# Kernel optimization log

Hardware: AMD Instinct MI355X
Metric: run time of the kernel (lower is better)

## Reference

```python
import jax, jax.numpy as jnp
import numpy as np

B, N, K, TC = 4, 4096, 16, 3
N_TAYLOR = 20  # 3rd-order Taylor monomials of (x,y,z): 1 + 3 + 6 + 10
CHANNELS = [(6, 32), (32, 64), (64, 128), (128, 256)]


def _taylor(rel):
    # rel: B,3,N,K relative coords -> B,20,N,K monomial basis up to degree 3
    x, y, z = rel[:, 0], rel[:, 1], rel[:, 2]
    one = jnp.ones_like(x)
    return jnp.stack([one, x, y, z,
                      x * x, x * y, x * z, y * y, y * z, z * z,
                      x * x * x, x * x * y, x * x * z, x * y * y, x * y * z,
                      x * z * z, y * y * y, y * y * z, y * z * z, z * z * z], axis=1)


def _group(feat, idx):
    # feat: B,C,N ; idx: B,N,K (int) -> B,C,N,K gathered neighbor features
    return jax.vmap(lambda f, i: f[:, i])(feat, idx)


def setup_inputs() -> dict:
    key = jax.random.key(0)
    ks = jax.random.split(key, 8)
    inp = {"pc": jax.random.normal(ks[0], (B, N, 6), dtype=jnp.float32)}
    for l, (cin, cout) in enumerate(CHANNELS, start=1):
        k1, k2 = jax.random.split(ks[l], 2)
        inp[f"w1_{l}"] = jax.random.normal(k1, (TC, N_TAYLOR), dtype=jnp.float32) * 0.1
        inp[f"b1_{l}"] = jnp.zeros((TC,), dtype=jnp.float32)
        fan_in = cin * TC * K
        inp[f"w2_{l}"] = jax.random.normal(k2, (cout, cin * TC, K), dtype=jnp.float32) * (1.0 / np.sqrt(fan_in))
        inp[f"b2_{l}"] = jnp.zeros((cout,), dtype=jnp.float32)
    return inp


def _forward(pc, params):
    pcT = pc.transpose(0, 2, 1)                 # B,6,N
    xyz = pcT[:, :3]                            # B,3,N
    # KNN graph: pairwise squared distances, top-k nearest (includes self)
    sq = jnp.sum(xyz * xyz, axis=1)             # B,N
    d2 = sq[:, :, None] + sq[:, None, :] - 2.0 * jnp.einsum('bcn,bcm->bnm', xyz, xyz)
    _, idx = jax.lax.top_k(-d2, K)              # B,N,K
    gxyz = _group(xyz, idx)                     # B,3,N,K
    rel = gxyz - xyz[:, :, :, None]             # B,3,N,K relative neighbor coords
    tay_basis = _taylor(rel)                    # B,20,N,K

    feat = pcT
    feats = []
    for (w1, b1, w2, b2) in params:
        # Taylor kernel weights: 1x1 conv over the 20 monomials -> TC channels
        tay = jnp.einsum('btnk,ct->bcnk', tay_basis, w1) + b1[None, :, None, None]  # B,TC,N,K
        gf = _group(feat, idx)                  # B,C,N,K
        C = gf.shape[1]
        fused = (gf[:, :, None] * tay[:, None]).reshape(B, C * TC, N, K)  # outer product
        # Conv2d(C*TC, out, kernel=(1,K)): contract channel and neighbor axes
        out = jnp.einsum('bcnk,ock->bon', fused, w2) + b2[None, :, None]
        feat = jax.nn.relu(out)                 # B,Cout,N
        feats.append(feat)

    point_feat = jnp.concatenate(feats, axis=1)  # B,480,N
    top2, _ = jax.lax.top_k(point_feat, 2)       # top-2 over N (last axis) -> B,480,2
    cat_feat = top2.reshape(B, -1)               # B,960
    return cat_feat, point_feat


def reference(pc, w1_1, b1_1, w2_1, b2_1, w1_2, b1_2, w2_2, b2_2,
              w1_3, b1_3, w2_3, b2_3, w1_4, b1_4, w2_4, b2_4):
    params = [(w1_1, b1_1, w2_1, b2_1), (w1_2, b1_2, w2_2, b2_2),
              (w1_3, b1_3, w2_3, b2_3), (w1_4, b1_4, w2_4, b2_4)]
    return _forward(pc, params)
```

## Files before the change

### kernel.cpp

```cpp
#include <hip/hip_runtime.h>
#include <hip/hip_fp16.h>
#include <cfloat>

#define BB 4
#define NN 4096
#define KK 16
#define NPTS (BB * NN)
#define NT48 (48 * NPTS)

typedef __attribute__((ext_vector_type(8))) _Float16 f16x8;
typedef __attribute__((ext_vector_type(4))) float f32x4;
typedef unsigned int u32;
typedef unsigned long long u64;

__device__ __forceinline__ short f2h(float v) {
  __half h = __float2half_rn(v);
  return __half_as_short(h);
}
__device__ __forceinline__ u32 mulh2(u32 a, __half2 t) {
  __half2 x = __hmul2(*(__half2*)&a, t);
  return *(u32*)&x;
}

__global__ __launch_bounds__(256) void pc2ft_kernel(const float* __restrict__ pc,
                                                    short* __restrict__ ft0,
                                                    float4* __restrict__ xyzq) {
  const int i = blockIdx.x * 256 + threadIdx.x;
  if (i >= NPTS) return;
  const float* s = pc + (size_t)i * 6;
  short* d = ft0 + (size_t)i * 8;
#pragma unroll
  for (int c = 0; c < 6; ++c) d[c] = f2h(s[c]);
  d[6] = 0; d[7] = 0;
  const float x = s[0], y = s[1], z = s[2];
  xyzq[i] = make_float4(x, y, z, fmaf(z, z, fmaf(y, y, x * x)));
}

__global__ __launch_bounds__(256) void knn_select(const float4* __restrict__ xyzq,
                                                  int* __restrict__ idx_out) {
  __shared__ float wT[4];
  __shared__ u64 list[128];
  __shared__ int lcnt;
  const int g = blockIdx.x;
  const int b = g >> 12;
  const int t = threadIdx.x;
  const int lane = t & 63;
  const float4* base = xyzq + (b << 12);
  const float4 q = xyzq[g];
  float d2v[16];
  float mymin = FLT_MAX;
#pragma unroll
  for (int i = 0; i < 16; ++i) {
    const float4 c = base[i * 256 + t];
    const float dot = fmaf(q.z, c.z, fmaf(q.y, c.y, q.x * c.x));
    d2v[i] = fmaf(-2.0f, dot, q.w + c.w);
    mymin = fminf(mymin, d2v[i]);
  }
  if (t == 0) lcnt = 0;
  float v = mymin;
#pragma unroll
  for (int k = 2; k <= 64; k <<= 1) {
#pragma unroll
    for (int j = k >> 1; j >= 1; j >>= 1) {
      const float o = __shfl_xor(v, j, 64);
      const bool take_min = (((lane & k) == 0) == ((lane & j) == 0));
      v = take_min ? fminf(v, o) : fmaxf(v, o);
    }
  }
  const float tw = __shfl(v, 15, 64);
  if (lane == 0) wT[t >> 6] = tw;
  __syncthreads();
  const float T = fminf(fminf(wT[0], wT[1]), fminf(wT[2], wT[3]));
#pragma unroll
  for (int i = 0; i < 16; ++i) {
    if (d2v[i] <= T) {
      const u32 bits = __float_as_uint(d2v[i]);
      const u32 key = bits ^ ((u32)((int)bits >> 31) | 0x80000000u);
      const int pos = atomicAdd(&lcnt, 1);
      if (pos < 128) list[pos] = ((u64)key << 32) | (u32)(i * 256 + t);
    }
  }
  __syncthreads();
  if (t < 128) {
    const int m = min(lcnt, 128);
    const u64 my = (t < m) ? list[t] : ~0ull;
    int rank = 0;
#pragma unroll 4
    for (int i = 0; i < m; ++i) rank += (list[i] < my) ? 1 : 0;
    if (t < m && rank < 16)
      idx_out[(size_t)g * KK + rank] = (int)(my & 0xFFFFFFFFull);
  }
}

__global__ __launch_bounds__(256) void wcvt_kernel(const float* __restrict__ w2,
                                                   short* __restrict__ wb,
                                                   int CIN, int COUT, int CPAD, int LOGC,
                                                   int total8) {
  const int i = blockIdx.x * 256 + threadIdx.x;
  if (i >= total8) return;
  const int q8 = i * 8;
  const int QT = CPAD * 48;
  const int o = q8 / QT;
  const int r = q8 - o * QT;
  const int kq = r >> LOGC;
  const int c0 = r & (CPAD - 1);
  const int tt = kq >> 4;
  const int k = kq & 15;
  short h[8];
#pragma unroll
  for (int j = 0; j < 8; ++j) {
    const int c = c0 + j;
    const float v = (o < COUT && c < CIN) ? w2[(size_t)o * CIN * 48 + (c * 3 + tt) * 16 + k] : 0.0f;
    h[j] = f2h(v);
  }
  short* d = wb + (size_t)o * QT + r;
#pragma unroll
  for (int j = 0; j < 8; ++j) d[j] = h[j];
}

__global__ __launch_bounds__(256) void taylor_kernel(
    const float* __restrict__ pc, const int* __restrict__ idx,
    const float* __restrict__ w1_1, const float* __restrict__ b1_1,
    const float* __restrict__ w1_2, const float* __restrict__ b1_2,
    const float* __restrict__ w1_3, const float* __restrict__ b1_3,
    const float* __restrict__ w1_4, const float* __restrict__ b1_4,
    float* __restrict__ tayg) {
  const int i = blockIdx.x * 256 + threadIdx.x;
  if (i >= NPTS * KK) return;
  const int p = i & (NPTS - 1);
  const int k = i >> 14;
  const int n = p & (NN - 1);
  const int b = p >> 12;
  const float* pcb = pc + (size_t)b * NN * 6;
  const int m = idx[(size_t)p * KK + k];
  const float x = pcb[m * 6 + 0] - pcb[n * 6 + 0];
  const float y = pcb[m * 6 + 1] - pcb[n * 6 + 1];
  const float z = pcb[m * 6 + 2] - pcb[n * 6 + 2];
  float tb[20];
  tb[0] = 1.0f; tb[1] = x; tb[2] = y; tb[3] = z;
  tb[4] = x * x; tb[5] = x * y; tb[6] = x * z;
  tb[7] = y * y; tb[8] = y * z; tb[9] = z * z;
  tb[10] = tb[4] * x; tb[11] = tb[4] * y; tb[12] = tb[4] * z;
  tb[13] = tb[5] * y; tb[14] = tb[5] * z; tb[15] = tb[6] * z;
  tb[16] = tb[7] * y; tb[17] = tb[7] * z; tb[18] = tb[8] * z; tb[19] = tb[9] * z;
  const float* w1s[4] = {w1_1, w1_2, w1_3, w1_4};
  const float* b1s[4] = {b1_1, b1_2, b1_3, b1_4};
#pragma unroll
  for (int l = 0; l < 4; ++l) {
    const float* w1 = w1s[l];
    const float* b1 = b1s[l];
#pragma unroll
    for (int c = 0; c < 3; ++c) {
      float s = b1[c];
#pragma unroll
      for (int j = 0; j < 20; ++j) s = fmaf(w1[c * 20 + j], tb[j], s);
      tayg[(size_t)(l * 48 + c * 16 + k) * NPTS + p] = s;
    }
  }
}

template <int CPAD, int LOGC, int COUT, int OTILE>
__global__ __launch_bounds__(256) void conv_mfma_kernel(
    const char* __restrict__ ftin,
    const short* __restrict__ wb,
    const float* __restrict__ b2,
    const float* __restrict__ tayg,
    const int* __restrict__ idx,
    float* __restrict__ pfout, int pfbstride,
    short* __restrict__ ftout, int CPADN) {
  constexpr int QTOT = CPAD * 48;
  constexpr int STEPS = QTOT / 32;
  constexpr int NJ = OTILE / 64;
  constexpr int PW = 16 * NJ;
  __shared__ __align__(16) short As[2][OTILE * 32];
  __shared__ __align__(16) short Bs[2][64 * 32];
  __shared__ __align__(16) float tayS[48 * 64];
  __shared__ int idxS[16 * 64];
  const int t = threadIdx.x;
  const int pbase = blockIdx.x * 64;
  const int obase = blockIdx.y * OTILE;
  const int b = pbase >> 12;
  const int nbase = pbase & (NN - 1);
  const int p_loc = t >> 2;
  const int sub = t & 3;
#pragma unroll
  for (int i = 0; i < 3; ++i) {
    const int f = i * 1024 + t * 4;
    *(float4*)&tayS[f] = *(const float4*)&tayg[(size_t)(f >> 6) * NPTS + pbase + (f & 63)];
  }
  {
    const int4 mi = *(const int4*)&idx[(size_t)(pbase + p_loc) * KK + sub * 4];
    const int gb = b << 12;
    idxS[(sub * 4 + 0) * 64 + p_loc] = (gb + mi.x) << (LOGC + 1);
    idxS[(sub * 4 + 1) * 64 + p_loc] = (gb + mi.y) << (LOGC + 1);
    idxS[(sub * 4 + 2) * 64 + p_loc] = (gb + mi.z) << (LOGC + 1);
    idxS[(sub * 4 + 3) * 64 + p_loc] = (gb + mi.w) << (LOGC + 1);
  }
  const int lane = t & 63;
  const int w = t >> 6;
  const int wm = (NJ == 2) ? (w & 1) : 0;
  const int wn = (NJ == 2) ? (w >> 1) : w;
  const int fr = lane & 15;
  const int fk = lane >> 4;
  const short* aw = wb + (size_t)(obase + p_loc) * QTOT + sub * 8;
  f32x4 acc[4][NJ];
#pragma unroll
  for (int i = 0; i < 4; ++i)
#pragma unroll
    for (int j = 0; j < NJ; ++j) acc[i][j] = (f32x4)(0.0f);
  __syncthreads();

  uint4 fv[2];
  float tv[2];
  auto pref = [&](int ss, int slot) {
    const int seg = ss * 32 + sub * 8;
    const int kq = seg >> LOGC;
    const int c0 = seg & (CPAD - 1);
    const int moff = idxS[(kq & 15) * 64 + p_loc];
    tv[slot] = tayS[kq * 64 + p_loc];
    fv[slot] = *(const uint4*)(ftin + moff + (c0 << 1));
  };
  auto build = [&](int slot, int dstph) {
    const __half2 t2 = __half2half2(__float2half_rn(tv[slot]));
    const uint4 f = fv[slot];
    uint4 r;
    r.x = mulh2(f.x, t2); r.y = mulh2(f.y, t2);
    r.z = mulh2(f.z, t2); r.w = mulh2(f.w, t2);
    const int chunk = sub ^ ((p_loc >> 1) & 3);
    *(uint4*)&Bs[dstph][p_loc * 32 + chunk * 8] = r;
  };
  auto dmaA = [&](int ss, int dstph) {
#pragma unroll
    for (int h = 0; h < NJ; ++h)
      __builtin_amdgcn_global_load_lds(
          (const __attribute__((address_space(1))) u32*)(aw + (size_t)h * 64 * QTOT + ss * 32),
          (__attribute__((address_space(3))) u32*)&As[dstph][h * 2048 + t * 8], 16, 0, 0);
  };
  pref(0, 0);
  dmaA(0, 0);
  pref(1, 1);
  build(0, 0);
  __syncthreads();
#pragma unroll 2
  for (int s = 0; s < STEPS; ++s) {
    const int ph = s & 1;
    if (s + 2 < STEPS) pref(s + 2, s & 1);
    if (s + 1 < STEPS) dmaA(s + 1, ph ^ 1);
    f16x8 af[4];
#pragma unroll
    for (int i = 0; i < 4; ++i)
      af[i] = *(const f16x8*)&As[ph][(wm * 64 + i * 16 + fr) * 32 + fk * 8];
    f16x8 bfr[NJ];
    const int bch = (fk ^ ((fr >> 1) & 3)) * 8;
#pragma unroll
    for (int j = 0; j < NJ; ++j)
      bfr[j] = *(const f16x8*)&Bs[ph][(wn * PW + j * 16 + fr) * 32 + bch];
    if (s + 1 < STEPS) build((s + 1) & 1, ph ^ 1);
#pragma unroll
    for (int i = 0; i < 4; ++i)
#pragma unroll
      for (int j = 0; j < NJ; ++j)
        acc[i][j] = __builtin_amdgcn_mfma_f32_16x16x32_f16(af[i], bfr[j], acc[i][j], 0, 0, 0);
    if (s + 1 < STEPS) __syncthreads();
  }
  float* outb = pfout + (size_t)b * pfbstride;
#pragma unroll
  for (int i = 0; i < 4; ++i) {
    const int o0 = obase + wm * 64 + i * 16 + fk * 4;
    if (o0 < COUT) {
      const float4 b4 = *(const float4*)&b2[o0];
#pragma unroll
      for (int j = 0; j < NJ; ++j) {
        const int p_l = wn * PW + j * 16 + fr;
        const float v0 = fmaxf(acc[i][j][0] + b4.x, 0.0f);
        const float v1 = fmaxf(acc[i][j][1] + b4.y, 0.0f);
        const float v2 = fmaxf(acc[i][j][2] + b4.z, 0.0f);
        const float v3 = fmaxf(acc[i][j][3] + b4.w, 0.0f);
        outb[(size_t)(o0 + 0) * NN + nbase + p_l] = v0;
        outb[(size_t)(o0 + 1) * NN + nbase + p_l] = v1;
        outb[(size_t)(o0 + 2) * NN + nbase + p_l] = v2;
        outb[(size_t)(o0 + 3) * NN + nbase + p_l] = v3;
        if (ftout) {
          const __half2 h01 = __floats2half2_rn(v0, v1);
          const __half2 h23 = __floats2half2_rn(v2, v3);
          uint2 pk;
          pk.x = *(const u32*)&h01;
          pk.y = *(const u32*)&h23;
          *(uint2*)&ftout[(size_t)(pbase + p_l) * CPADN + o0] = pk;
        }
      }
    }
  }
}

__global__ __launch_bounds__(256) void top2_kernel(const float* __restrict__ pf,
                                                   float* __restrict__ cat) {
  const int row = blockIdx.x;
  const float* p = pf + (size_t)row * NN;
  float m1 = -FLT_MAX, m2 = -FLT_MAX;
  for (int i = threadIdx.x; i < NN; i += 256) {
    const float v = p[i];
    if (v > m1) { m2 = m1; m1 = v; }
    else if (v > m2) m2 = v;
  }
#pragma unroll
  for (int off = 32; off > 0; off >>= 1) {
    const float o1 = __shfl_down(m1, off, 64);
    const float o2 = __shfl_down(m2, off, 64);
    const float nm1 = fmaxf(m1, o1);
    const float nm2 = fmaxf(fminf(m1, o1), fmaxf(m2, o2));
    m1 = nm1; m2 = nm2;
  }
  __shared__ float s1[4], s2[4];
  const int wid = threadIdx.x >> 6;
  if ((threadIdx.x & 63) == 0) { s1[wid] = m1; s2[wid] = m2; }
  __syncthreads();
  if (threadIdx.x == 0) {
    m1 = s1[0]; m2 = s2[0];
#pragma unroll
    for (int w = 1; w < 4; ++w) {
      const float o1 = s1[w], o2 = s2[w];
      const float nm1 = fmaxf(m1, o1);
      const float nm2 = fmaxf(fminf(m1, o1), fmaxf(m2, o2));
      m1 = nm1; m2 = nm2;
    }
    const int b = row / 480, ch = row % 480;
    cat[b * 960 + ch * 2 + 0] = m1;
    cat[b * 960 + ch * 2 + 1] = m2;
  }
}

extern "C" void kernel_launch(void* const* d_in, const int* in_sizes, int n_in,
                              void* d_out, int out_size, void* d_ws, size_t ws_size,
                              hipStream_t stream) {
  const float* pc = (const float*)d_in[0];
  const float* w1s[4]; const float* b1s[4]; const float* w2s[4]; const float* b2s[4];
  for (int l = 0; l < 4; ++l) {
    w1s[l] = (const float*)d_in[1 + 4 * l];
    b1s[l] = (const float*)d_in[2 + 4 * l];
    w2s[l] = (const float*)d_in[3 + 4 * l];
    b2s[l] = (const float*)d_in[4 + 4 * l];
  }
  char* W = (char*)d_ws;
  int* idx = (int*)W;
  float* tayg = (float*)(W + 1048576);
  short* wb1 = (short*)(W + 13631488);
  short* wb2 = wb1 + 64 * 384;
  short* wb3 = wb2 + 64 * 1536;
  short* wb4 = wb3 + 128 * 3072;
  short* ft0 = (short*)(W + 17809408);
  short* ft1 = (short*)(W + 18071552);
  float4* xyzq = (float4*)(W + 1048576);
  short* ft2 = (short*)(W + 1048576);
  short* ft3 = (short*)(W + 1048576 + 2097152);
  float* cat = (float*)d_out;
  float* pf = (float*)d_out + BB * 960;
  const int pfstride = 480 * NN;

  pc2ft_kernel<<<dim3(NPTS / 256), 256, 0, stream>>>(pc, ft0, xyzq);
  knn_select<<<dim3(NPTS), 256, 0, stream>>>(xyzq, idx);
  wcvt_kernel<<<dim3((64 * 384 / 8 + 255) / 256), 256, 0, stream>>>(w2s[0], wb1, 6, 32, 8, 3, 64 * 384 / 8);
  wcvt_kernel<<<dim3((64 * 1536 / 8 + 255) / 256), 256, 0, stream>>>(w2s[1], wb2, 32, 64, 32, 5, 64 * 1536 / 8);
  wcvt_kernel<<<dim3((128 * 3072 / 8 + 255) / 256), 256, 0, stream>>>(w2s[2], wb3, 64, 128, 64, 6, 128 * 3072 / 8);
  wcvt_kernel<<<dim3((256 * 6144 / 8 + 255) / 256), 256, 0, stream>>>(w2s[3], wb4, 128, 256, 128, 7, 256 * 6144 / 8);
  taylor_kernel<<<dim3(NPTS * KK / 256), 256, 0, stream>>>(
      pc, idx, w1s[0], b1s[0], w1s[1], b1s[1], w1s[2], b1s[2], w1s[3], b1s[3], tayg);
  conv_mfma_kernel<8, 3, 32, 64><<<dim3(NPTS / 64, 1), 256, 0, stream>>>(
      (const char*)ft0, wb1, b2s[0], tayg + 0 * (size_t)NT48, idx,
      pf + (size_t)0 * NN, pfstride, ft1, 32);
  conv_mfma_kernel<32, 5, 64, 64><<<dim3(NPTS / 64, 1), 256, 0, stream>>>(
      (const char*)ft1, wb2, b2s[1], tayg + 1 * (size_t)NT48, idx,
      pf + (size_t)32 * NN, pfstride, ft2, 64);
  conv_mfma_kernel<64, 6, 128, 64><<<dim3(NPTS / 64, 2), 256, 0, stream>>>(
      (const char*)ft2, wb3, b2s[2], tayg + 2 * (size_t)NT48, idx,
      pf + (size_t)96 * NN, pfstride, ft3, 128);
  conv_mfma_kernel<128, 7, 256, 128><<<dim3(NPTS / 64, 2), 256, 0, stream>>>(
      (const char*)ft3, wb4, b2s[3], tayg + 3 * (size_t)NT48, idx,
      pf + (size_t)224 * NN, pfstride, nullptr, 0);
  top2_kernel<<<dim3(BB * 480), 256, 0, stream>>>(pf, cat);
}
```

Measured before the change: 377.1 us.

## Feed MFMA operands directly from registers, removing LDS staging and block barriers

New measurement: 600.0 us. 1.59x slower.

```diff
diff --git a/kernel.cpp b/kernel.cpp
--- a/kernel.cpp
+++ b/kernel.cpp
@@ -160,7 +160,7 @@
 }
 
 template <int CPAD, int LOGC, int COUT, int OTILE>
-__global__ __launch_bounds__(256) void conv_mfma_kernel(
+__global__ __launch_bounds__(256) void conv_reg_kernel(
     const char* __restrict__ ftin,
     const short* __restrict__ wb,
     const float* __restrict__ b2,
@@ -172,8 +172,6 @@
   constexpr int STEPS = QTOT / 32;
   constexpr int NJ = OTILE / 64;
   constexpr int PW = 16 * NJ;
-  __shared__ __align__(16) short As[2][OTILE * 32];
-  __shared__ __align__(16) short Bs[2][64 * 32];
   __shared__ __align__(16) float tayS[48 * 64];
   __shared__ int idxS[16 * 64];
   const int t = threadIdx.x;
@@ -181,14 +179,14 @@
   const int obase = blockIdx.y * OTILE;
   const int b = pbase >> 12;
   const int nbase = pbase & (NN - 1);
-  const int p_loc = t >> 2;
-  const int sub = t & 3;
 #pragma unroll
   for (int i = 0; i < 3; ++i) {
     const int f = i * 1024 + t * 4;
     *(float4*)&tayS[f] = *(const float4*)&tayg[(size_t)(f >> 6) * NPTS + pbase + (f & 63)];
   }
   {
+    const int p_loc = t >> 2;
+    const int sub = t & 3;
     const int4 mi = *(const int4*)&idx[(size_t)(pbase + p_loc) * KK + sub * 4];
     const int gb = b << 12;
     idxS[(sub * 4 + 0) * 64 + p_loc] = (gb + mi.x) << (LOGC + 1);
@@ -202,7 +200,11 @@
   const int wn = (NJ == 2) ? (w >> 1) : w;
   const int fr = lane & 15;
   const int fk = lane >> 4;
-  const short* aw = wb + (size_t)(obase + p_loc) * QTOT + sub * 8;
+  const int fkx8 = fk * 8;
+  const short* awbase = wb + (size_t)(obase + wm * 64 + fr) * QTOT + fkx8;
+  int pl[NJ];
+#pragma unroll
+  for (int j = 0; j < NJ; ++j) pl[j] = wn * PW + j * 16 + fr;
   f32x4 acc[4][NJ];
 #pragma unroll
   for (int i = 0; i < 4; ++i)
@@ -210,58 +212,45 @@
     for (int j = 0; j < NJ; ++j) acc[i][j] = (f32x4)(0.0f);
   __syncthreads();
 
-  uint4 fv[2];
-  float tv[2];
-  auto pref = [&](int ss, int slot) {
-    const int seg = ss * 32 + sub * 8;
-    const int kq = seg >> LOGC;
-    const int c0 = seg & (CPAD - 1);
-    const int moff = idxS[(kq & 15) * 64 + p_loc];
-    tv[slot] = tayS[kq * 64 + p_loc];
-    fv[slot] = *(const uint4*)(ftin + moff + (c0 << 1));
+  uint4 areg[2][4];
+  uint4 bfv[2][NJ];
+  float btv[2][NJ];
+  auto loadstep = [&](int s, int slot) {
+    const int q0 = s * 32 + fkx8;
+    const int kq = q0 >> LOGC;
+    const int c0 = q0 & (CPAD - 1);
+#pragma unroll
+    for (int i = 0; i < 4; ++i)
+      areg[slot][i] = *(const uint4*)(awbase + (size_t)i * 16 * QTOT + s * 32);
+#pragma unroll
+    for (int j = 0; j < NJ; ++j) {
+      const int moff = idxS[(kq & 15) * 64 + pl[j]];
+      btv[slot][j] = tayS[kq * 64 + pl[j]];
+      bfv[slot][j] = *(const uint4*)(ftin + moff + (c0 << 1));
+    }
   };
-  auto build = [&](int slot, int dstph) {
-    const __half2 t2 = __half2half2(__float2half_rn(tv[slot]));
-    const uint4 f = fv[slot];
-    uint4 r;
-    r.x = mulh2(f.x, t2); r.y = mulh2(f.y, t2);
-    r.z = mulh2(f.z, t2); r.w = mulh2(f.w, t2);
-    const int chunk = sub ^ ((p_loc >> 1) & 3);
-    *(uint4*)&Bs[dstph][p_loc * 32 + chunk * 8] = r;
-  };
-  auto dmaA = [&](int ss, int dstph) {
-#pragma unroll
-    for (int h = 0; h < NJ; ++h)
-      __builtin_amdgcn_global_load_lds(
-          (const __attribute__((address_space(1))) u32*)(aw + (size_t)h * 64 * QTOT + ss * 32),
-          (__attribute__((address_space(3))) u32*)&As[dstph][h * 2048 + t * 8], 16, 0, 0);
-  };
-  pref(0, 0);
-  dmaA(0, 0);
-  pref(1, 1);
-  build(0, 0);
-  __syncthreads();
+  loadstep(0, 0);
 #pragma unroll 2
   for (int s = 0; s < STEPS; ++s) {
-    const int ph = s & 1;
-    if (s + 2 < STEPS) pref(s + 2, s & 1);
-    if (s + 1 < STEPS) dmaA(s + 1, ph ^ 1);
-    f16x8 af[4];
-#pragma unroll
-    for (int i = 0; i < 4; ++i)
-      af[i] = *(const f16x8*)&As[ph][(wm * 64 + i * 16 + fr) * 32 + fk * 8];
+    const int cur = s & 1;
+    if (s + 1 < STEPS) loadstep(s + 1, cur ^ 1);
     f16x8 bfr[NJ];
-    const int bch = (fk ^ ((fr >> 1) & 3)) * 8;
-#pragma unroll
-    for (int j = 0; j < NJ; ++j)
-      bfr[j] = *(const f16x8*)&Bs[ph][(wn * PW + j * 16 + fr) * 32 + bch];
-    if (s + 1 < STEPS) build((s + 1) & 1, ph ^ 1);
-#pragma unroll
-    for (int i = 0; i < 4; ++i)
+#pragma unroll
+    for (int j = 0; j < NJ; ++j) {
+      const __half2 t2 = __half2half2(__float2half_rn(btv[cur][j]));
+      const uint4 f = bfv[cur][j];
+      uint4 r;
+      r.x = mulh2(f.x, t2); r.y = mulh2(f.y, t2);
+      r.z = mulh2(f.z, t2); r.w = mulh2(f.w, t2);
+      bfr[j] = *(const f16x8*)&r;
+    }
+#pragma unroll
+    for (int i = 0; i < 4; ++i) {
+      const f16x8 af = *(const f16x8*)&areg[cur][i];
 #pragma unroll
       for (int j = 0; j < NJ; ++j)
-        acc[i][j] = __builtin_amdgcn_mfma_f32_16x16x32_f16(af[i], bfr[j], acc[i][j], 0, 0, 0);
-    if (s + 1 < STEPS) __syncthreads();
+        acc[i][j] = __builtin_amdgcn_mfma_f32_16x16x32_f16(af, bfr[j], acc[i][j], 0, 0, 0);
+    }
   }
   float* outb = pfout + (size_t)b * pfbstride;
 #pragma unroll
@@ -271,7 +260,7 @@
       const float4 b4 = *(const float4*)&b2[o0];
 #pragma unroll
       for (int j = 0; j < NJ; ++j) {
-        const int p_l = wn * PW + j * 16 + fr;
+        const int p_l = pl[j];
         const float v0 = fmaxf(acc[i][j][0] + b4.x, 0.0f);
         const float v1 = fmaxf(acc[i][j][1] + b4.y, 0.0f);
         const float v2 = fmaxf(acc[i][j][2] + b4.z, 0.0f);
@@ -365,16 +354,16 @@
   wcvt_kernel<<<dim3((256 * 6144 / 8 + 255) / 256), 256, 0, stream>>>(w2s[3], wb4, 128, 256, 128, 7, 256 * 6144 / 8);
   taylor_kernel<<<dim3(NPTS * KK / 256), 256, 0, stream>>>(
       pc, idx, w1s[0], b1s[0], w1s[1], b1s[1], w1s[2], b1s[2], w1s[3], b1s[3], tayg);
-  conv_mfma_kernel<8, 3, 32, 64><<<dim3(NPTS / 64, 1), 256, 0, stream>>>(
+  conv_reg_kernel<8, 3, 32, 64><<<dim3(NPTS / 64, 1), 256, 0, stream>>>(
       (const char*)ft0, wb1, b2s[0], tayg + 0 * (size_t)NT48, idx,
       pf + (size_t)0 * NN, pfstride, ft1, 32);
-  conv_mfma_kernel<32, 5, 64, 64><<<dim3(NPTS / 64, 1), 256, 0, stream>>>(
+  conv_reg_kernel<32, 5, 64, 64><<<dim3(NPTS / 64, 1), 256, 0, stream>>>(
       (const char*)ft1, wb2, b2s[1], tayg + 1 * (size_t)NT48, idx,
       pf + (size_t)32 * NN, pfstride, ft2, 64);
-  conv_mfma_kernel<64, 6, 128, 64><<<dim3(NPTS / 64, 2), 256, 0, stream>>>(
+  conv_reg_kernel<64, 6, 128, 64><<<dim3(NPTS / 64, 2), 256, 0, stream>>>(
       (const char*)ft2, wb3, b2s[2], tayg + 2 * (size_t)NT48, idx,
       pf + (size_t)96 * NN, pfstride, ft3, 128);
-  conv_mfma_kernel<128, 7, 256, 128><<<dim3(NPTS / 64, 2), 256, 0, stream>>>(
+  conv_reg_kernel<128, 7, 256, 128><<<dim3(NPTS / 64, 2), 256, 0, stream>>>(
       (const char*)ft3, wb4, b2s[3], tayg + 3 * (size_t)NT48, idx,
       pf + (size_t)224 * NN, pfstride, nullptr, 0);
   top2_kernel<<<dim3(BB * 480), 256, 0, stream>>>(pf, cat);
```

## Double K-step per iteration in conv MFMA loop with swizzled 64-wide LDS tiles

Applied to the files above, without the earlier changes.

After: 367.6 us. 1.03x faster.

```diff
diff --git a/kernel.cpp b/kernel.cpp
--- a/kernel.cpp
+++ b/kernel.cpp
@@ -169,12 +169,13 @@
     float* __restrict__ pfout, int pfbstride,
     short* __restrict__ ftout, int CPADN) {
   constexpr int QTOT = CPAD * 48;
-  constexpr int STEPS = QTOT / 32;
+  constexpr int OUTER = QTOT / 64;
   constexpr int NJ = OTILE / 64;
   constexpr int PW = 16 * NJ;
-  __shared__ __align__(16) short As[2][OTILE * 32];
-  __shared__ __align__(16) short Bs[2][64 * 32];
-  __shared__ __align__(16) float tayS[48 * 64];
+  constexpr int NH = OTILE / 32;
+  __shared__ __align__(16) short As[2][OTILE * 64];
+  __shared__ __align__(16) short Bs[2][64 * 64];
+  __shared__ __align__(16) unsigned short tayH[48 * 64];
   __shared__ int idxS[16 * 64];
   const int t = threadIdx.x;
   const int pbase = blockIdx.x * 64;
@@ -186,7 +187,13 @@
 #pragma unroll
   for (int i = 0; i < 3; ++i) {
     const int f = i * 1024 + t * 4;
-    *(float4*)&tayS[f] = *(const float4*)&tayg[(size_t)(f >> 6) * NPTS + pbase + (f & 63)];
+    const float4 tv4 = *(const float4*)&tayg[(size_t)(f >> 6) * NPTS + pbase + (f & 63)];
+    ushort4 h4;
+    h4.x = (unsigned short)f2h(tv4.x);
+    h4.y = (unsigned short)f2h(tv4.y);
+    h4.z = (unsigned short)f2h(tv4.z);
+    h4.w = (unsigned short)f2h(tv4.w);
+    *(ushort4*)&tayH[f] = h4;
   }
   {
     const int4 mi = *(const int4*)&idx[(size_t)(pbase + p_loc) * KK + sub * 4];
@@ -196,72 +203,86 @@
     idxS[(sub * 4 + 2) * 64 + p_loc] = (gb + mi.z) << (LOGC + 1);
     idxS[(sub * 4 + 3) * 64 + p_loc] = (gb + mi.w) << (LOGC + 1);
   }
+  const int arow = t >> 3;
+  const int apos = t & 7;
+  const int aswz = (t >> 4) & 7;
+  const short* awl[NH];
+#pragma unroll
+  for (int h = 0; h < NH; ++h)
+    awl[h] = wb + (size_t)(obase + h * 32 + arow) * QTOT + ((apos ^ aswz) * 8);
+  auto dmaA = [&](int o, int ph) {
+#pragma unroll
+    for (int h = 0; h < NH; ++h)
+      __builtin_amdgcn_global_load_lds(
+          (const __attribute__((address_space(1))) u32*)(awl[h] + o * 64),
+          (__attribute__((address_space(3))) u32*)&As[ph][h * 2048 + t * 8], 16, 0, 0);
+  };
   const int lane = t & 63;
   const int w = t >> 6;
   const int wm = (NJ == 2) ? (w & 1) : 0;
   const int wn = (NJ == 2) ? (w >> 1) : w;
   const int fr = lane & 15;
   const int fk = lane >> 4;
-  const short* aw = wb + (size_t)(obase + p_loc) * QTOT + sub * 8;
+  const int rsw = (fr >> 1) & 7;
+  const int bswz = (p_loc >> 1) & 7;
   f32x4 acc[4][NJ];
 #pragma unroll
   for (int i = 0; i < 4; ++i)
 #pragma unroll
     for (int j = 0; j < NJ; ++j) acc[i][j] = (f32x4)(0.0f);
+
+  uint4 fv[2];
+  unsigned short tvh[2];
+  auto prefB = [&](int o) {
+#pragma unroll
+    for (int z = 0; z < 2; ++z) {
+      const int q0 = o * 64 + z * 32 + sub * 8;
+      const int kq = q0 >> LOGC;
+      const int c0 = q0 & (CPAD - 1);
+      const int moff = idxS[(kq & 15) * 64 + p_loc];
+      tvh[z] = tayH[kq * 64 + p_loc];
+      fv[z] = *(const uint4*)(ftin + moff + (c0 << 1));
+    }
+  };
+  auto buildB = [&](int ph) {
+#pragma unroll
+    for (int z = 0; z < 2; ++z) {
+      const __half2 t2 = __half2half2(__ushort_as_half(tvh[z]));
+      const uint4 f = fv[z];
+      uint4 r;
+      r.x = mulh2(f.x, t2); r.y = mulh2(f.y, t2);
+      r.z = mulh2(f.z, t2); r.w = mulh2(f.w, t2);
+      const int pos = (z * 4 + sub) ^ bswz;
+      *(uint4*)&Bs[ph][p_loc * 64 + pos * 8] = r;
+    }
+  };
+  dmaA(0, 0);
   __syncthreads();
-
-  uint4 fv[2];
-  float tv[2];
-  auto pref = [&](int ss, int slot) {
-    const int seg = ss * 32 + sub * 8;
-    const int kq = seg >> LOGC;
-    const int c0 = seg & (CPAD - 1);
-    const int moff = idxS[(kq & 15) * 64 + p_loc];
-    tv[slot] = tayS[kq * 64 + p_loc];
-    fv[slot] = *(const uint4*)(ftin + moff + (c0 << 1));
-  };
-  auto build = [&](int slot, int dstph) {
-    const __half2 t2 = __half2half2(__float2half_rn(tv[slot]));
-    const uint4 f = fv[slot];
-    uint4 r;
-    r.x = mulh2(f.x, t2); r.y = mulh2(f.y, t2);
-    r.z = mulh2(f.z, t2); r.w = mulh2(f.w, t2);
-    const int chunk = sub ^ ((p_loc >> 1) & 3);
-    *(uint4*)&Bs[dstph][p_loc * 32 + chunk * 8] = r;
-  };
-  auto dmaA = [&](int ss, int dstph) {
-#pragma unroll
-    for (int h = 0; h < NJ; ++h)
-      __builtin_amdgcn_global_load_lds(
-          (const __attribute__((address_space(1))) u32*)(aw + (size_t)h * 64 * QTOT + ss * 32),
-          (__attribute__((address_space(3))) u32*)&As[dstph][h * 2048 + t * 8], 16, 0, 0);
-  };
-  pref(0, 0);
-  dmaA(0, 0);
-  pref(1, 1);
-  build(0, 0);
+  prefB(0);
+  buildB(0);
   __syncthreads();
-#pragma unroll 2
-  for (int s = 0; s < STEPS; ++s) {
-    const int ph = s & 1;
-    if (s + 2 < STEPS) pref(s + 2, s & 1);
-    if (s + 1 < STEPS) dmaA(s + 1, ph ^ 1);
-    f16x8 af[4];
-#pragma unroll
-    for (int i = 0; i < 4; ++i)
-      af[i] = *(const f16x8*)&As[ph][(wm * 64 + i * 16 + fr) * 32 + fk * 8];
-    f16x8 bfr[NJ];
-    const int bch = (fk ^ ((fr >> 1) & 3)) * 8;
-#pragma unroll
-    for (int j = 0; j < NJ; ++j)
-      bfr[j] = *(const f16x8*)&Bs[ph][(wn * PW + j * 16 + fr) * 32 + bch];
-    if (s + 1 < STEPS) build((s + 1) & 1, ph ^ 1);
-#pragma unroll
-    for (int i = 0; i < 4; ++i)
+#pragma unroll 1
+  for (int o = 0; o < OUTER; ++o) {
+    const int ph = o & 1;
+    if (o + 1 < OUTER) { dmaA(o + 1, ph ^ 1); prefB(o + 1); }
+#pragma unroll
+    for (int z = 0; z < 2; ++z) {
+      f16x8 af[4], bf[NJ];
+      const int pos8 = ((z * 4 + fk) ^ rsw) * 8;
+#pragma unroll
+      for (int i = 0; i < 4; ++i)
+        af[i] = *(const f16x8*)&As[ph][(wm * 64 + i * 16 + fr) * 64 + pos8];
 #pragma unroll
       for (int j = 0; j < NJ; ++j)
-        acc[i][j] = __builtin_amdgcn_mfma_f32_16x16x32_f16(af[i], bfr[j], acc[i][j], 0, 0, 0);
-    if (s + 1 < STEPS) __syncthreads();
+        bf[j] = *(const f16x8*)&Bs[ph][(wn * PW + j * 16 + fr) * 64 + pos8];
+#pragma unroll
+      for (int i = 0; i < 4; ++i)
+#pragma unroll
+        for (int j = 0; j < NJ; ++j)
+          acc[i][j] = __builtin_amdgcn_mfma_f32_16x16x32_f16(af[i], bf[j], acc[i][j], 0, 0, 0);
+      if (z == 0 && o + 1 < OUTER) buildB(ph ^ 1);
+    }
+    if (o + 1 < OUTER) __syncthreads();
   }
   float* outb = pfout + (size_t)b * pfbstride;
 #pragma unroll
```
